# Performance work log

Measured on AMD Instinct MI355X. Metric: run time of the kernel, lower is better.

Reference implementation:

```python
import jax, jax.numpy as jnp
import numpy as np

B, C, H, W = 4, 256, 64, 64
CH = C // 2


def setup_inputs() -> dict:
    key = jax.random.key(0)
    ks = jax.random.split(key, 8)
    s_in = 1.0 / np.sqrt(C)  # conv2d default init scale (fan_in = C for 1x1)
    return {
        "a": jax.random.normal(ks[0], (B, C, H, W), dtype=jnp.float32),
        "p": jax.random.normal(ks[1], (B, C, H, W), dtype=jnp.float32),
        "Wq": jax.random.uniform(ks[2], (CH, C), jnp.float32, -s_in, s_in),
        "bq": jax.random.uniform(ks[3], (CH,), jnp.float32, -s_in, s_in),
        "Wk": jax.random.uniform(ks[4], (CH, C), jnp.float32, -s_in, s_in),
        "bk": jax.random.uniform(ks[5], (CH,), jnp.float32, -s_in, s_in),
        "Wv": jax.random.uniform(ks[6], (C, C), jnp.float32, -s_in, s_in),
        "bv": jax.random.uniform(ks[7], (C,), jnp.float32, -s_in, s_in),
    }


def reference(a, p, Wq, bq, Wk, bk, Wv, bv):
    b, c, h, w = a.shape
    hw = h * w
    # 1x1 convs == per-pixel channel matmuls; flatten spatial dims to hw
    Q = jnp.einsum('oc,bchw->bohw', Wq, a).reshape(b, -1, hw) + bq[None, :, None]   # [B, C/2, HW]
    K = jnp.einsum('oc,bchw->bohw', Wk, p).reshape(b, -1, hw) + bk[None, :, None]   # [B, C/2, HW]
    V = jnp.einsum('oc,bchw->bohw', Wv, p).reshape(b, -1, hw) + bv[None, :, None]   # [B, C,   HW]
    # attn[b,m,n] = softmax_n( Q[:, :, m] . K[:, :, n] )
    attn = jax.nn.softmax(jnp.einsum('bcm,bcn->bmn', Q, K), axis=-1)                # [B, HW, HW]
    # out[b,c,m] = sum_n V[b,c,n] * attn[b,m,n]  (V @ attn^T)
    out = jnp.einsum('bcn,bmn->bcm', V, attn).reshape(b, c, h, w)
    return out + a
```

## Files before the change

### kernel.cpp

```cpp
#include <hip/hip_runtime.h>
#include <stdint.h>

#define B_ 4
#define C_ 256
#define CH_ 128
#define HW_ 4096
#define L2E 1.44269504f
#define SHIFT_L2 14.4269504f

typedef __bf16 bf16;
typedef __bf16 v8bf __attribute__((ext_vector_type(8)));
typedef __bf16 v4bf __attribute__((ext_vector_type(4)));
typedef float v4f __attribute__((ext_vector_type(4)));
struct f4 { float x, y, z, w; };

#define GAS __attribute__((address_space(1)))
#define LAS __attribute__((address_space(3)))

__device__ __forceinline__ void async_copy16(const void* gptr, void* lptr) {
  __builtin_amdgcn_global_load_lds((GAS void*)gptr, (LAS void*)lptr, 16, 0, 0);
}

__global__ __launch_bounds__(512)
void proj_kernel(const float* __restrict__ a, const float* __restrict__ p,
                 const float* __restrict__ Wq, const float* __restrict__ bq,
                 const float* __restrict__ Wk, const float* __restrict__ bk,
                 const float* __restrict__ Wv, const float* __restrict__ bv,
                 bf16* __restrict__ Qt, bf16* __restrict__ Kt, bf16* __restrict__ Vn)
{
  __shared__ bf16 Xt[64 * 272];
  __shared__ bf16 Ds[9216];

  const int t = threadIdx.x;
  const int lane = t & 63;
  const int w = t >> 6;
  const int l15 = lane & 15;
  const int q = lane >> 4;

  const int s0 = blockIdx.x * 64;
  const int b = blockIdx.y;
  const int z = blockIdx.z;

  const float* X = (z == 0) ? a : p;
  const float* W; const float* bias;
  if (z == 0)      { W = Wq; bias = bq; }
  else if (z == 1) { W = Wk; bias = bk; }
  else             { W = Wv + (size_t)(z - 2) * 128 * C_; bias = bv + (z - 2) * 128; }

  const float* Xb = X + ((size_t)b * C_) * HW_;
  for (int j = 0; j < 16; ++j) {
    int linear = t + 512 * j;
    int s = linear & 63;
    int cp = linear >> 6;
    float x0 = Xb[(size_t)(2 * cp) * HW_ + s0 + s];
    float x1 = Xb[(size_t)(2 * cp + 1) * HW_ + s0 + s];
    unsigned short u0 = __builtin_bit_cast(unsigned short, (bf16)x0);
    unsigned short u1 = __builtin_bit_cast(unsigned short, (bf16)x1);
    *(unsigned int*)&Xt[s * 272 + 2 * cp] = (unsigned int)u0 | ((unsigned int)u1 << 16);
  }

  v8bf Af[8];
  const float* Wrow = W + (size_t)(16 * w + l15) * C_;
  #pragma unroll
  for (int kk = 0; kk < 8; ++kk) {
    f4 f0 = *(const f4*)&Wrow[kk * 32 + q * 8];
    f4 f1 = *(const f4*)&Wrow[kk * 32 + q * 8 + 4];
    v8bf f;
    f[0] = (bf16)f0.x; f[1] = (bf16)f0.y; f[2] = (bf16)f0.z; f[3] = (bf16)f0.w;
    f[4] = (bf16)f1.x; f[5] = (bf16)f1.y; f[6] = (bf16)f1.z; f[7] = (bf16)f1.w;
    Af[kk] = f;
  }

  __syncthreads();

  v4f acc[4];
  #pragma unroll
  for (int ns = 0; ns < 4; ++ns) { v4f zz = {0.f, 0.f, 0.f, 0.f}; acc[ns] = zz; }
  #pragma unroll
  for (int ns = 0; ns < 4; ++ns)
    #pragma unroll
    for (int kk = 0; kk < 8; ++kk) {
      v8bf Bf = *(const v8bf*)&Xt[(16 * ns + l15) * 272 + kk * 32 + q * 8];
      acc[ns] = __builtin_amdgcn_mfma_f32_16x16x32_bf16(Af[kk], Bf, acc[ns], 0, 0, 0);
    }

  if (z < 2) {
    #pragma unroll
    for (int ns = 0; ns < 4; ++ns)
      #pragma unroll
      for (int r = 0; r < 4; ++r)
        Ds[(16 * ns + l15) * 144 + 16 * w + 4 * q + r] =
            (bf16)(acc[ns][r] + bias[16 * w + 4 * q + r]);
    __syncthreads();
    bf16* dst = (z == 0) ? Qt : Kt;
    #pragma unroll
    for (int i = 0; i < 2; ++i) {
      int idx = t + 512 * i;
      int s = idx >> 4, ch = (idx & 15) * 8;
      *(v8bf*)&dst[((size_t)b * HW_ + s0 + s) * CH_ + ch] = *(const v8bf*)&Ds[s * 144 + ch];
    }
  } else {
    int o0 = (z - 2) * 128;
    #pragma unroll
    for (int ns = 0; ns < 4; ++ns)
      #pragma unroll
      for (int r = 0; r < 4; ++r) {
        int pos = 32 * (ns >> 1) + 8 * (l15 >> 2) + 4 * (ns & 1) + (l15 & 3);
        Ds[(16 * w + 4 * q + r) * 72 + pos] =
            (bf16)(acc[ns][r] + bias[16 * w + 4 * q + r]);
      }
    __syncthreads();
    #pragma unroll
    for (int i = 0; i < 2; ++i) {
      int idx = t + 512 * i;
      int o = idx >> 3, ch = (idx & 7) * 8;
      *(v8bf*)&Vn[((size_t)b * C_ + o0 + o) * HW_ + s0 + ch] = *(const v8bf*)&Ds[o * 72 + ch];
    }
  }
}

#define LDS_V 16640
#define TSTRIDE 52
#define TREGION 13312
#define LDS_TOTAL 53248

__global__ __launch_bounds__(256, 2)
void attn_kernel(const bf16* __restrict__ Qt, const bf16* __restrict__ Kt,
                 const bf16* __restrict__ Vn, const float* __restrict__ a,
                 float* __restrict__ out, bf16* __restrict__ Op,
                 float* __restrict__ Ls, int nsplit)
{
  extern __shared__ char smem[];
  const int t = threadIdx.x;
  const int lane = t & 63;
  const int w = t >> 6;
  const int l15 = lane & 15;
  const int q = lane >> 4;
  const int b = blockIdx.y;
  const int sp = blockIdx.z;
  const int m0 = blockIdx.x * 128;

  v8bf Qf[2][4];
  #pragma unroll
  for (int s = 0; s < 2; ++s) {
    const bf16* qrow = Qt + ((size_t)b * HW_ + m0 + 32 * w + 16 * s + l15) * CH_;
    #pragma unroll
    for (int kk = 0; kk < 4; ++kk)
      Qf[s][kk] = *(const v8bf*)&qrow[kk * 32 + q * 8];
  }

  v4f O[2][16];
  #pragma unroll
  for (int s = 0; s < 2; ++s)
    #pragma unroll
    for (int cs = 0; cs < 16; ++cs) { v4f zz = {0.f, 0.f, 0.f, 0.f}; O[s][cs] = zz; }
  float lsum[2] = {0.f, 0.f};

  const bf16* Kb = Kt + (size_t)b * HW_ * CH_;
  const bf16* Vb = Vn + (size_t)b * C_ * HW_;

  const int NT = 64 / nsplit;
  const int t0 = sp * NT;

  auto stageK = [&](int n0) {
    #pragma unroll
    for (int j = 0; j < 4; ++j) {
      int i = 4 * j + w;
      async_copy16(Kb + ((size_t)(n0 + i + 16 * q)) * CH_ + l15 * 8, smem + i * 1040);
    }
  };
  auto stageV = [&](int n0) {
    #pragma unroll
    for (int j = 0; j < 8; ++j) {
      int i = 4 * j + w;
      async_copy16(Vb + ((size_t)(i + 32 * (lane >> 3))) * HW_ + n0 + (lane & 7) * 8,
                   smem + LDS_V + i * 1040);
    }
  };

  stageK(t0 * 64);
  stageV(t0 * 64);
  __syncthreads();

  for (int nt = 0; nt < NT; ++nt) {
    int n0 = (t0 + nt) * 64;

    v4f St[4][2];
    #pragma unroll
    for (int sub = 0; sub < 4; ++sub)
      #pragma unroll
      for (int s = 0; s < 2; ++s) { v4f zz = {0.f, 0.f, 0.f, 0.f}; St[sub][s] = zz; }
    #pragma unroll
    for (int sub = 0; sub < 4; ++sub)
      #pragma unroll
      for (int kk = 0; kk < 4; ++kk) {
        v8bf Kf = *(const v8bf*)(smem + l15 * 1040 + sub * 256 + kk * 64 + q * 16);
        St[sub][0] = __builtin_amdgcn_mfma_f32_16x16x32_bf16(Kf, Qf[0][kk], St[sub][0], 0, 0, 0);
        St[sub][1] = __builtin_amdgcn_mfma_f32_16x16x32_bf16(Kf, Qf[1][kk], St[sub][1], 0, 0, 0);
      }

    __syncthreads();
    if (nt + 1 < NT) stageK(n0 + 64);

    v8bf Pf[2][2];
    #pragma unroll
    for (int s = 0; s < 2; ++s) {
      float ls = 0.f;
      #pragma unroll
      for (int kk = 0; kk < 2; ++kk)
        #pragma unroll
        for (int a2 = 0; a2 < 2; ++a2)
          #pragma unroll
          for (int r = 0; r < 4; ++r) {
            float pv = exp2f(St[2 * kk + a2][s][r] * L2E - SHIFT_L2);
            Pf[s][kk][4 * a2 + r] = (bf16)pv;
            ls += pv;
          }
      lsum[s] += ls;
    }

    #pragma unroll
    for (int cs = 0; cs < 16; ++cs)
      #pragma unroll
      for (int kk = 0; kk < 2; ++kk) {
        v8bf Vf = *(const v8bf*)(smem + LDS_V +
                                 (16 * (cs & 1) + l15) * 1040 + (cs >> 1) * 128 + kk * 64 + q * 16);
        O[0][cs] = __builtin_amdgcn_mfma_f32_16x16x32_bf16(Pf[0][kk], Vf, O[0][cs], 0, 0, 0);
        O[1][cs] = __builtin_amdgcn_mfma_f32_16x16x32_bf16(Pf[1][kk], Vf, O[1][cs], 0, 0, 0);
      }

    __syncthreads();
    if (nt + 1 < NT) stageV(n0 + 64);
  }

  float lfin[2];
  #pragma unroll
  for (int s = 0; s < 2; ++s) {
    float l = lsum[s];
    l += __shfl_xor(l, 16);
    l += __shfl_xor(l, 32);
    lfin[s] = l;
  }

  if (nsplit > 1 && lane < 16) {
    #pragma unroll
    for (int s = 0; s < 2; ++s)
      Ls[((size_t)sp * B_ + b) * HW_ + m0 + 32 * w + 16 * s + lane] = lfin[s];
  }

  float linv[2][4];
  #pragma unroll
  for (int s = 0; s < 2; ++s)
    #pragma unroll
    for (int r = 0; r < 4; ++r)
      linv[s][r] = (nsplit == 1) ? 1.0f / __shfl(lfin[s], 4 * q + r) : 1.0f;

  bf16* T = (bf16*)smem;
  for (int round = 0; round < 2; ++round) {
    __syncthreads();
    if ((w >> 1) == round) {
      bf16* Tw = T + (w & 1) * TREGION;
      #pragma unroll
      for (int s = 0; s < 2; ++s)
        #pragma unroll
        for (int cs = 0; cs < 16; ++cs) {
          v4bf pp4;
          #pragma unroll
          for (int r = 0; r < 4; ++r) pp4[r] = (bf16)(O[s][cs][r] * linv[s][r]);
          *(v4bf*)&Tw[(16 * cs + l15) * TSTRIDE + 16 * s + 4 * q] = pp4;
        }
    }
    __syncthreads();
    #pragma unroll
    for (int it = 0; it < 8; ++it) {
      int idx = t + 256 * it;
      int tt = idx >> 10;
      int c = (idx >> 2) & 255;
      int mc = idx & 3;
      int wavew = round * 2 + tt;
      int mg = m0 + 32 * wavew + mc * 8;
      const bf16* Trow = &T[tt * TREGION + c * TSTRIDE + mc * 8];
      v4bf lo = *(const v4bf*)&Trow[0];
      v4bf hi = *(const v4bf*)&Trow[4];
      if (nsplit == 1) {
        size_t gi = ((size_t)b * C_ + c) * HW_ + mg;
        #pragma unroll
        for (int j2 = 0; j2 < 4; ++j2) out[gi + j2] = (float)lo[j2] + a[gi + j2];
        #pragma unroll
        for (int j2 = 0; j2 < 4; ++j2) out[gi + 4 + j2] = (float)hi[j2] + a[gi + 4 + j2];
      } else {
        size_t gi = (((size_t)sp * B_ + b) * C_ + c) * HW_ + mg;
        v8bf val;
        #pragma unroll
        for (int j2 = 0; j2 < 4; ++j2) { val[j2] = lo[j2]; val[4 + j2] = hi[j2]; }
        *(v8bf*)&Op[gi] = val;
      }
    }
  }
}

__global__ __launch_bounds__(256)
void combine_kernel(const bf16* __restrict__ Op, const float* __restrict__ Ls,
                    const float* __restrict__ a, float* __restrict__ out, int nsplit)
{
  int idx = blockIdx.x * 256 + threadIdx.x;
  int m4 = (idx & (HW_ / 4 - 1)) * 4;
  int bc = idx >> 10;
  int b = bc >> 8;

  float a0 = 0.f, a1 = 0.f, a2 = 0.f, a3 = 0.f;
  float L0 = 0.f, L1 = 0.f, L2 = 0.f, L3 = 0.f;
  for (int s = 0; s < nsplit; ++s) {
    v4bf o = *(const v4bf*)&Op[((size_t)s * B_ * C_ + bc) * HW_ + m4];
    f4 lp = *(const f4*)&Ls[((size_t)s * B_ + b) * HW_ + m4];
    a0 += (float)o[0]; a1 += (float)o[1]; a2 += (float)o[2]; a3 += (float)o[3];
    L0 += lp.x; L1 += lp.y; L2 += lp.z; L3 += lp.w;
  }
  f4 av = *(const f4*)&a[(size_t)bc * HW_ + m4];
  f4 ov;
  ov.x = a0 / L0 + av.x;
  ov.y = a1 / L1 + av.y;
  ov.z = a2 / L2 + av.z;
  ov.w = a3 / L3 + av.w;
  *(f4*)&out[(size_t)bc * HW_ + m4] = ov;
}

extern "C" void kernel_launch(void* const* d_in, const int* in_sizes, int n_in,
                              void* d_out, int out_size, void* d_ws, size_t ws_size,
                              hipStream_t stream) {
  const float* a  = (const float*)d_in[0];
  const float* p  = (const float*)d_in[1];
  const float* Wq = (const float*)d_in[2];
  const float* bq = (const float*)d_in[3];
  const float* Wk = (const float*)d_in[4];
  const float* bk = (const float*)d_in[5];
  const float* Wv = (const float*)d_in[6];
  const float* bv = (const float*)d_in[7];
  float* out = (float*)d_out;

  bf16* Qt = (bf16*)d_ws;
  bf16* Kt = Qt + (size_t)B_ * HW_ * CH_;
  bf16* Vn = Kt + (size_t)B_ * HW_ * CH_;

  const size_t proj_bytes = 16777216ull;
  const size_t part_bytes = (size_t)B_ * C_ * HW_ * 2;
  const size_t stat_bytes = (size_t)B_ * HW_ * 4;
  auto need = [&](int S) { return proj_bytes + (size_t)S * (part_bytes + stat_bytes); };

  int S;
  if      (ws_size >= need(4)) S = 4;
  else if (ws_size >= need(2)) S = 2;
  else                         S = 1;

  bf16* Op = (bf16*)((char*)d_ws + proj_bytes);
  float* Ls = (float*)((char*)d_ws + proj_bytes + (size_t)S * part_bytes);

  dim3 pg(HW_ / 64, B_, 4);
  proj_kernel<<<pg, 512, 0, stream>>>(a, p, Wq, bq, Wk, bk, Wv, bv, Qt, Kt, Vn);

  dim3 ag(HW_ / 128, B_, S);
  attn_kernel<<<ag, 256, LDS_TOTAL, stream>>>(Qt, Kt, Vn, a, out, Op, Ls, S);

  if (S > 1) {
    int nblk = (B_ * C_ * HW_ / 4) / 256;
    combine_kernel<<<nblk, 256, 0, stream>>>(Op, Ls, a, out, S);
  }
}
```

Baseline: 174.7 us.

## Double-buffer K/V tiles, enlarge attention blocks to 512 threads, remap grid for L2 locality

The attention kernel now uses two LDS buffers so the next K and V tile loads are issued at the start of each iteration and overlap with the current MFMA work. This removes one barrier per iteration. Blocks grow to 512 threads covering 256 query rows, and block indices are remapped so that blocks resident together share the same batch and split, which should improve L2 reuse of K/V. The projection kernel's input transpose now loads float2 pairs. In exchange the kernel needs about 100KB of LDS per block, which limits occupancy and requires raising the dynamic shared memory attribute.

```diff
diff --git a/kernel.cpp b/kernel.cpp
--- a/kernel.cpp
+++ b/kernel.cpp
@@ -13,6 +13,7 @@
 typedef __bf16 v4bf __attribute__((ext_vector_type(4)));
 typedef float v4f __attribute__((ext_vector_type(4)));
 struct f4 { float x, y, z, w; };
+struct f2 { float x, y; };
 
 #define GAS __attribute__((address_space(1)))
 #define LAS __attribute__((address_space(3)))
@@ -48,15 +49,19 @@
   else             { W = Wv + (size_t)(z - 2) * 128 * C_; bias = bv + (z - 2) * 128; }
 
   const float* Xb = X + ((size_t)b * C_) * HW_;
-  for (int j = 0; j < 16; ++j) {
+  #pragma unroll
+  for (int j = 0; j < 8; ++j) {
     int linear = t + 512 * j;
-    int s = linear & 63;
-    int cp = linear >> 6;
-    float x0 = Xb[(size_t)(2 * cp) * HW_ + s0 + s];
-    float x1 = Xb[(size_t)(2 * cp + 1) * HW_ + s0 + s];
-    unsigned short u0 = __builtin_bit_cast(unsigned short, (bf16)x0);
-    unsigned short u1 = __builtin_bit_cast(unsigned short, (bf16)x1);
-    *(unsigned int*)&Xt[s * 272 + 2 * cp] = (unsigned int)u0 | ((unsigned int)u1 << 16);
+    int s = (linear & 31) * 2;
+    int cp = linear >> 5;
+    f2 x0 = *(const f2*)&Xb[(size_t)(2 * cp) * HW_ + s0 + s];
+    f2 x1 = *(const f2*)&Xb[(size_t)(2 * cp + 1) * HW_ + s0 + s];
+    unsigned short u00 = __builtin_bit_cast(unsigned short, (bf16)x0.x);
+    unsigned short u01 = __builtin_bit_cast(unsigned short, (bf16)x0.y);
+    unsigned short u10 = __builtin_bit_cast(unsigned short, (bf16)x1.x);
+    unsigned short u11 = __builtin_bit_cast(unsigned short, (bf16)x1.y);
+    *(unsigned int*)&Xt[(s + 0) * 272 + 2 * cp] = (unsigned int)u00 | ((unsigned int)u10 << 16);
+    *(unsigned int*)&Xt[(s + 1) * 272 + 2 * cp] = (unsigned int)u01 | ((unsigned int)u11 << 16);
   }
 
   v8bf Af[8];
@@ -119,12 +124,14 @@
   }
 }
 
+#define BUFSZ 49920
+#define LDS_K 0
 #define LDS_V 16640
 #define TSTRIDE 52
 #define TREGION 13312
-#define LDS_TOTAL 53248
-
-__global__ __launch_bounds__(256, 2)
+#define LDS_TOTAL 99840
+
+__global__ __launch_bounds__(512, 2)
 void attn_kernel(const bf16* __restrict__ Qt, const bf16* __restrict__ Kt,
                  const bf16* __restrict__ Vn, const float* __restrict__ a,
                  float* __restrict__ out, bf16* __restrict__ Op,
@@ -136,9 +143,14 @@
   const int w = t >> 6;
   const int l15 = lane & 15;
   const int q = lane >> 4;
-  const int b = blockIdx.y;
-  const int sp = blockIdx.z;
-  const int m0 = blockIdx.x * 128;
+
+  const int Lhw = blockIdx.x + 16 * (blockIdx.y + 4 * blockIdx.z);
+  const int cpx = 8 * nsplit;
+  const int logical = (Lhw & 7) * cpx + (Lhw >> 3);
+  const int m0 = (logical & 15) * 256;
+  const int gg = logical >> 4;
+  const int b = gg & 3;
+  const int sp = gg >> 2;
 
   v8bf Qf[2][4];
   #pragma unroll
@@ -162,28 +174,31 @@
   const int NT = 64 / nsplit;
   const int t0 = sp * NT;
 
-  auto stageK = [&](int n0) {
+  auto stage = [&](int tile, int bsel) {
+    char* base = smem + bsel * BUFSZ;
+    int n0 = tile * 64;
+    #pragma unroll
+    for (int j = 0; j < 2; ++j) {
+      int i = 8 * j + w;
+      async_copy16(Kb + ((size_t)(n0 + i + 16 * q)) * CH_ + l15 * 8, base + LDS_K + i * 1040);
+    }
     #pragma unroll
     for (int j = 0; j < 4; ++j) {
-      int i = 4 * j + w;
-      async_copy16(Kb + ((size_t)(n0 + i + 16 * q)) * CH_ + l15 * 8, smem + i * 1040);
+      int i = 8 * j + w;
+      async_copy16(Vb + ((size_t)(i + 32 * (lane >> 3))) * HW_ + n0 + (lane & 7) * 8,
+                   base + LDS_V + i * 1040);
     }
   };
-  auto stageV = [&](int n0) {
-    #pragma unroll
-    for (int j = 0; j < 8; ++j) {
-      int i = 4 * j + w;
-      async_copy16(Vb + ((size_t)(i + 32 * (lane >> 3))) * HW_ + n0 + (lane & 7) * 8,
-                   smem + LDS_V + i * 1040);
-    }
-  };
-
-  stageK(t0 * 64);
-  stageV(t0 * 64);
+
+  stage(t0, 0);
   __syncthreads();
 
+  int cur = 0;
   for (int nt = 0; nt < NT; ++nt) {
-    int n0 = (t0 + nt) * 64;
+    if (nt + 1 < NT) stage(t0 + nt + 1, cur ^ 1);
+
+    const char* Kbase = smem + cur * BUFSZ + LDS_K;
+    const char* Vbase = smem + cur * BUFSZ + LDS_V;
 
     v4f St[4][2];
     #pragma unroll
@@ -194,13 +209,10 @@
     for (int sub = 0; sub < 4; ++sub)
       #pragma unroll
       for (int kk = 0; kk < 4; ++kk) {
-        v8bf Kf = *(const v8bf*)(smem + l15 * 1040 + sub * 256 + kk * 64 + q * 16);
+        v8bf Kf = *(const v8bf*)(Kbase + l15 * 1040 + sub * 256 + kk * 64 + q * 16);
         St[sub][0] = __builtin_amdgcn_mfma_f32_16x16x32_bf16(Kf, Qf[0][kk], St[sub][0], 0, 0, 0);
         St[sub][1] = __builtin_amdgcn_mfma_f32_16x16x32_bf16(Kf, Qf[1][kk], St[sub][1], 0, 0, 0);
       }
-
-    __syncthreads();
-    if (nt + 1 < NT) stageK(n0 + 64);
 
     v8bf Pf[2][2];
     #pragma unroll
@@ -223,14 +235,14 @@
     for (int cs = 0; cs < 16; ++cs)
       #pragma unroll
       for (int kk = 0; kk < 2; ++kk) {
-        v8bf Vf = *(const v8bf*)(smem + LDS_V +
+        v8bf Vf = *(const v8bf*)(Vbase +
                                  (16 * (cs & 1) + l15) * 1040 + (cs >> 1) * 128 + kk * 64 + q * 16);
         O[0][cs] = __builtin_amdgcn_mfma_f32_16x16x32_bf16(Pf[0][kk], Vf, O[0][cs], 0, 0, 0);
         O[1][cs] = __builtin_amdgcn_mfma_f32_16x16x32_bf16(Pf[1][kk], Vf, O[1][cs], 0, 0, 0);
       }
 
     __syncthreads();
-    if (nt + 1 < NT) stageV(n0 + 64);
+    cur ^= 1;
   }
 
   float lfin[2];
@@ -256,7 +268,7 @@
       linv[s][r] = (nsplit == 1) ? 1.0f / __shfl(lfin[s], 4 * q + r) : 1.0f;
 
   bf16* T = (bf16*)smem;
-  for (int round = 0; round < 2; ++round) {
+  for (int round = 0; round < 4; ++round) {
     __syncthreads();
     if ((w >> 1) == round) {
       bf16* Tw = T + (w & 1) * TREGION;
@@ -272,8 +284,8 @@
     }
     __syncthreads();
     #pragma unroll
-    for (int it = 0; it < 8; ++it) {
-      int idx = t + 256 * it;
+    for (int it = 0; it < 4; ++it) {
+      int idx = t + 512 * it;
       int tt = idx >> 10;
       int c = (idx >> 2) & 255;
       int mc = idx & 3;
@@ -355,11 +367,18 @@
   bf16* Op = (bf16*)((char*)d_ws + proj_bytes);
   float* Ls = (float*)((char*)d_ws + proj_bytes + (size_t)S * part_bytes);
 
+  static bool attr_done = false;
+  if (!attr_done) {
+    hipFuncSetAttribute((const void*)attn_kernel,
+                        hipFuncAttributeMaxDynamicSharedMemorySize, LDS_TOTAL);
+    attr_done = true;
+  }
+
   dim3 pg(HW_ / 64, B_, 4);
   proj_kernel<<<pg, 512, 0, stream>>>(a, p, Wq, bq, Wk, bk, Wv, bv, Qt, Kt, Vn);
 
-  dim3 ag(HW_ / 128, B_, S);
-  attn_kernel<<<ag, 256, LDS_TOTAL, stream>>>(Qt, Kt, Vn, a, out, Op, Ls, S);
+  dim3 ag(HW_ / 256, B_, S);
+  attn_kernel<<<ag, 512, LDS_TOTAL, stream>>>(Qt, Kt, Vn, a, out, Op, Ls, S);
 
   if (S > 1) {
     int nblk = (B_ * C_ * HW_ / 4) / 256;
```

After: 174.0 us. Within noise of the previous version (-0.4%).
